# Optimization experiments

Hardware: AMD Instinct MI355X
Metric: run time of the kernel (lower is better)

Reference implementation:

```python
import jax, jax.numpy as jnp
import numpy as np

B, T, F, N = 262144, 3, 17, 8
EMBD = 32
DT = 0.2  # 25/5*0.04
EPS = 1e-8  # torch.cosine_similarity eps


def _mono(x, wi, bi, wo, bo):
    # monotonic_fun with increasing=False: relu(-Linear(x)) -> Linear
    h = jax.nn.relu(-(x @ wi.T + bi))  # (..., EMBD)
    return h @ wo.T + bo               # (..., 1)


def _cos(a, b):
    dot = jnp.sum(a * b, axis=-1)
    na = jnp.maximum(jnp.linalg.norm(a, axis=-1), EPS)
    nb = jnp.maximum(jnp.linalg.norm(b, axis=-1), EPS)
    return dot / (na * nb)


def _angle_clamp(vec, e, ang):
    # vec: (B,K,2), e: (B,2) -> keep forces within effective angle cone, sum over K
    keep = jnp.abs(_cos(e[:, None, :], vec)) > ang
    return jnp.sum(vec * keep[..., None], axis=1)


def setup_inputs() -> dict:
    key = jax.random.key(0)
    ks = jax.random.split(key, 8)
    ego = jax.random.normal(ks[0], (B, T, F), jnp.float32)
    ego = ego.at[:, :, 2:4].multiply(10.0)  # position scale
    nei = jax.random.normal(ks[1], (B, N, F), jnp.float32)
    nei = nei.at[:, :, 2:4].multiply(10.0).at[:, :, 4:6].multiply(0.1)
    border = jax.random.normal(ks[2], (4,), jnp.float32)
    attr_dest_para = jax.random.uniform(ks[3], (2,), jnp.float32) + 0.1  # relu(rand), keep away from 0 divisor
    eff_angle = jax.nn.sigmoid(jax.random.uniform(ks[4], (1,), jnp.float32))

    def mlp(k):
        k1, k2, k3, k4 = jax.random.split(k, 4)
        wi = jax.random.uniform(k1, (EMBD, 1), jnp.float32)      # clamped >= 0
        bi = jax.random.normal(k2, (EMBD,), jnp.float32) * 0.1
        wo = jax.random.uniform(k3, (1, EMBD), jnp.float32) * 0.1  # clamped >= 0
        bo = jax.random.normal(k4, (1,), jnp.float32) * 0.1
        return wi, bi, wo, bo

    an = mlp(ks[5])
    rn = mlp(ks[6])
    rb = mlp(ks[7])
    dl = mlp(jax.random.fold_in(key, 99))
    return dict(
        ego=ego, nei=nei, border=border,
        attr_dest_para=attr_dest_para, eff_angle=eff_angle,
        an_wi=an[0], an_bi=an[1], an_wo=an[2], an_bo=an[3],
        rn_wi=rn[0], rn_bi=rn[1], rn_wo=rn[2], rn_bo=rn[3],
        rb_wi=rb[0], rb_bi=rb[1], rb_wo=rb[2], rb_bo=rb[3],
        dl_wi=dl[0], dl_bi=dl[1], dl_wo=dl[2], dl_bo=dl[3],
    )


def reference(ego, nei, border, attr_dest_para, eff_angle,
              an_wi, an_bi, an_wo, an_bo,
              rn_wi, rn_bi, rn_wo, rn_bo,
              rb_wi, rb_bi, rb_wo, rb_bo,
              dl_wi, dl_bi, dl_wo, dl_bo):
    ego_last = ego[:, -1]  # (B,F)

    # --- attr_destination (desired_velocity=None branch) ---
    v34 = ego_last[:, 3:5]
    dv = jnp.stack([jnp.linalg.norm(v34, axis=-1),
                    jnp.zeros(ego.shape[0], ego.dtype)], axis=1)  # (B,2)
    f_dest = ((attr_dest_para[1] * dv - v34) / attr_dest_para[0])[:, None, :]  # (B,1,2)

    # --- attr_repu_neighbors ---
    r = nei[:, :, 2:4] - ego_last[:, None, 2:4]  # (B,N,2)
    mask = nei[:, :, 2:4] == 0                    # (B,N,2)
    r_norm = jnp.linalg.norm(r, axis=-1, keepdims=True)  # (B,N,1)

    # neighbor durality: quirky use of batch element 1, shared across batch
    ids_last = ego[1, -1, 8:-1]  # (8,) neighbor-id columns
    dur = jnp.zeros(N, ego.dtype)
    for t in range(ego.shape[1]):
        dur = dur + jnp.isin(ids_last, ego[1, t, 8:-1]).astype(ego.dtype)

    f_attr = _mono(r_norm, an_wi, an_bi, an_wo, an_bo) * r / r_norm \
             * _mono(dur[:, None], dl_wi, dl_bi, dl_wo, dl_bo)  # (B,N,2)*(N,1)
    f_attr = jnp.where(mask, 0.0, f_attr)

    v_nei = nei[:, :, 4:6]
    b = r_norm \
        + jnp.sum((r + v_nei * DT) ** 2, axis=-1, keepdims=True) \
        - jnp.sum((v_nei * DT) ** 2, axis=-1, keepdims=True)
    b = jnp.sqrt(b) / 2
    f_repu = _mono(b, rn_wi, rn_bi, rn_wo, rn_bo) * r / r_norm
    f_repu = jnp.where(mask, 0.0, f_repu)

    # --- repu_borders (select_lane = [0, -1]) ---
    rb_all = ego_last[:, 3, None] - border        # (B,4)
    rbv = jnp.stack([rb_all[:, 0], rb_all[:, -1]], axis=1)  # (B,2)
    rbn = jnp.abs(rbv)
    f_bor = _mono(rbn[..., None], rb_wi, rb_bi, rb_wo, rb_bo) * (rbv / rbn)[..., None]  # (B,2,1)
    f_bor = jnp.concatenate([jnp.zeros_like(f_bor), f_bor], axis=-1)  # (B,2,2): [0, fy]

    # --- angle clamp + integrate ---
    e = ego_last[:, 4:6]
    e = e / jnp.linalg.norm(e, axis=1, keepdims=True)
    a = (_angle_clamp(f_dest, e, eff_angle)
         + _angle_clamp(f_attr, e, eff_angle) + _angle_clamp(f_repu, e, eff_angle)
         + _angle_clamp(f_bor, e, eff_angle))
    v = ego_last[:, 2:4] + a * DT
    s = ego_last[:, :2] + v * DT
    return jnp.concatenate([s, v, a], axis=1)  # (B,6)
```

## Files before the change

### kernel.cpp

```cpp
#include <hip/hip_runtime.h>

#define DTC 0.2f
#define EPSC 1e-8f


__global__ __launch_bounds__(128) void sfm_pre(
    const float* __restrict__ ego,
    const float* __restrict__ an_wi, const float* __restrict__ an_bi, const float* __restrict__ an_wo,
    const float* __restrict__ rn_wi, const float* __restrict__ rn_bi, const float* __restrict__ rn_wo,
    const float* __restrict__ rb_wi, const float* __restrict__ rb_bi, const float* __restrict__ rb_wo,
    const float* __restrict__ dl_wi, const float* __restrict__ dl_bi,
    const float* __restrict__ dl_wo, const float* __restrict__ dl_bo,
    float* __restrict__ ws)
{
    __shared__ float tk[96], wiwo[96], wobi[96], skn[96], ssw[96], ssb[96];
    int t = threadIdx.x;
    if (t < 96) {
        int f = t >> 5, k = t & 31;
        const float* wip = (f == 0) ? an_wi : ((f == 1) ? rn_wi : rb_wi);
        const float* bip = (f == 0) ? an_bi : ((f == 1) ? rn_bi : rb_bi);
        const float* wop = (f == 0) ? an_wo : ((f == 1) ? rn_wo : rb_wo);
        float wi = wip[k], bi = bip[k], wo = wop[k];
        tk[t]   = -bi / wi;
        wiwo[t] = wi * wo;
        wobi[t] = wo * bi;
    }
    __syncthreads();
    if (t < 96) {
        int f = t >> 5, k = t & 31;
        float my = tk[t];
        int rank = 0;
        for (int m = 0; m < 32; ++m) {
            float o = tk[f * 32 + m];
            rank += (o < my || (o == my && m < k)) ? 1 : 0;
        }
        skn[f * 32 + rank] = my;
        ssw[f * 32 + rank] = wiwo[t];
        ssb[f * 32 + rank] = wobi[t];
    }
    __syncthreads();
    if (t < 96) {
        int f = t >> 5, p = t & 31;
        float sw_ = 0.f, sb_ = 0.f;
        for (int m = p; m < 32; ++m) { sw_ += ssw[f * 32 + m]; sb_ += ssb[f * 32 + m]; }
        int base = 16 + f * 112;
        ws[base + p]      = skn[f * 32 + p];
        ws[base + 32 + p] = sw_;
        ws[base + 65 + p] = sb_;
        if (p == 0) { ws[base + 64] = 0.f; ws[base + 97] = 0.f; }
    }
    if (t >= 96 && t < 104) {
        int j = t - 96;
        const float* base = ego + 51;
        float idv = base[2 * 17 + 8 + j];
        float dur = 0.f;
        for (int tt = 0; tt < 3; ++tt) {
            bool fo = false;
            for (int m = 0; m < 8; ++m) fo = fo || (idv == base[tt * 17 + 8 + m]);
            dur += fo ? 1.f : 0.f;
        }
        float acc = 0.f;
        for (int k = 0; k < 32; ++k)
            acc = fmaf(dl_wo[k], fmaxf(0.f, -fmaf(dl_wi[k], dur, dl_bi[k])), acc);
        ws[j] = acc + dl_bo[0];
    }
}

__device__ __forceinline__ float mono_eval(const float* __restrict__ kn, float x) {
    int i = (kn[15] <= x) ? 16 : 0;
    i += (kn[i + 7] <= x) ? 8 : 0;
    i += (kn[i + 3] <= x) ? 4 : 0;
    i += (kn[i + 1] <= x) ? 2 : 0;
    i += (kn[i] <= x) ? 1 : 0;
    return -fmaf(kn[32 + i], x, kn[65 + i]);
}

__global__ __launch_bounds__(256) void sfm_main(
    const float* __restrict__ ego, const float* __restrict__ nei,
    const float* __restrict__ border, const float* __restrict__ adp,
    const float* __restrict__ eang,
    const float* __restrict__ an_bo, const float* __restrict__ rn_bo,
    const float* __restrict__ rb_bo,
    const float* __restrict__ wsrc,
    float* __restrict__ out, int Bn)
{
    __shared__ float sw[360];
    int t = threadIdx.x;
    for (int i = t; i < 352; i += 256) sw[i] = wsrc[i];
    if (t == 0) sw[352] = an_bo[0];
    if (t == 1) sw[353] = rn_bo[0];
    if (t == 2) sw[354] = rb_bo[0];
    if (t == 3) sw[355] = adp[0];
    if (t == 4) sw[356] = adp[1];
    if (t == 5) sw[357] = eang[0];
    if (t == 6) sw[358] = border[0];
    if (t == 7) sw[359] = border[3];
    __syncthreads();

    int l = t & 7;
    long long row = (long long)blockIdx.x * 32 + (t >> 3);
    if (row >= Bn) return;

    float egv = 0.f;
    if (l < 6) egv = ego[row * 51 + 34 + l];
    int lb = (t & 63) & ~7;
    float g0 = __shfl(egv, lb + 0, 64);
    float g1 = __shfl(egv, lb + 1, 64);
    float g2 = __shfl(egv, lb + 2, 64);
    float g3 = __shfl(egv, lb + 3, 64);
    float g4 = __shfl(egv, lb + 4, 64);
    float g5 = __shfl(egv, lb + 5, 64);

    const float* nr = nei + row * 136 + l * 17 + 2;
    float nx = nr[0], ny = nr[1], vx = nr[2], vy = nr[3];

    float Rx = nx - g2, Ry = ny - g3;
    float rr = sqrtf(Rx * Rx + Ry * Ry);
    float ax = fmaf(vx, DTC, Rx), ay = fmaf(vy, DTC, Ry);
    float wx = vx * DTC, wy = vy * DTC;
    float bb = sqrtf(rr + ax * ax + ay * ay - wx * wx - wy * wy) * 0.5f;

    float an_bo_v = sw[352], rn_bo_v = sw[353], rb_bo_v = sw[354];
    float p0 = sw[355], p1 = sw[356], ang = sw[357];
    float rb0 = g3 - sw[358], rb1 = g3 - sw[359];
    float rbn0 = fabsf(rb0), rbn1 = fabsf(rb1);

    float fA = mono_eval(sw + 16, rr) + an_bo_v;
    float fR = mono_eval(sw + 128, bb) + rn_bo_v;
    float xb = (l == 1) ? rbn1 : rbn0;
    float vB = 0.f;
    if (l < 2) vB = mono_eval(sw + 240, xb) + rb_bo_v;
    float vB0 = __shfl(vB, lb + 0, 64);
    float vB1 = __shfl(vB, lb + 1, 64);

    float elen = sqrtf(g4 * g4 + g5 * g5);
    float ex = g4 / elen, ey = g5 / elen;
    float na = fmaxf(sqrtf(ex * ex + ey * ey), EPSC);

    float axs = 0.f, ays = 0.f;
#define CLAMP_ADD(VX, VY)                                                   \
    {                                                                       \
        float _vx = (VX), _vy = (VY);                                       \
        float _nv = fmaxf(sqrtf(_vx * _vx + _vy * _vy), EPSC);              \
        float _c = (ex * _vx + ey * _vy) / (na * _nv);                      \
        if (fabsf(_c) > ang) { axs += _vx; ays += _vy; }                    \
    }

    float mfx = (nx == 0.f) ? 0.f : 1.f;
    float mfy = (ny == 0.f) ? 0.f : 1.f;

    {
        float coef = fA / rr * sw[l];
        CLAMP_ADD(coef * Rx * mfx, coef * Ry * mfy);
    }
    {
        float coef = fR / rr;
        CLAMP_ADD(coef * Rx * mfx, coef * Ry * mfy);
    }

#pragma unroll
    for (int m = 1; m < 8; m <<= 1) {
        axs += __shfl_xor(axs, m, 64);
        ays += __shfl_xor(ays, m, 64);
    }

    if (l == 0) {
        float dvn = sqrtf(g3 * g3 + g4 * g4);
        CLAMP_ADD((p1 * dvn - g3) / p0, -g4 / p0);
        CLAMP_ADD(0.f, vB0 * (rb0 / rbn0));
        CLAMP_ADD(0.f, vB1 * (rb1 / rbn1));

        float vxo = fmaf(axs, DTC, g2);
        float vyo = fmaf(ays, DTC, g3);
        float* op = out + row * 6;
        op[0] = fmaf(vxo, DTC, g0);
        op[1] = fmaf(vyo, DTC, g1);
        op[2] = vxo; op[3] = vyo;
        op[4] = axs; op[5] = ays;
    }
#undef CLAMP_ADD
}

extern "C" void kernel_launch(void* const* d_in, const int* in_sizes, int n_in,
                              void* d_out, int out_size, void* d_ws, size_t ws_size,
                              hipStream_t stream) {
    const float* ego    = (const float*)d_in[0];
    const float* nei    = (const float*)d_in[1];
    const float* border = (const float*)d_in[2];
    const float* adp    = (const float*)d_in[3];
    const float* eang   = (const float*)d_in[4];
    const float* an_wi  = (const float*)d_in[5];
    const float* an_bi  = (const float*)d_in[6];
    const float* an_wo  = (const float*)d_in[7];
    const float* an_bo  = (const float*)d_in[8];
    const float* rn_wi  = (const float*)d_in[9];
    const float* rn_bi  = (const float*)d_in[10];
    const float* rn_wo  = (const float*)d_in[11];
    const float* rn_bo  = (const float*)d_in[12];
    const float* rb_wi  = (const float*)d_in[13];
    const float* rb_bi  = (const float*)d_in[14];
    const float* rb_wo  = (const float*)d_in[15];
    const float* rb_bo  = (const float*)d_in[16];
    const float* dl_wi  = (const float*)d_in[17];
    const float* dl_bi  = (const float*)d_in[18];
    const float* dl_wo  = (const float*)d_in[19];
    const float* dl_bo  = (const float*)d_in[20];
    float* out = (float*)d_out;
    float* ws  = (float*)d_ws;

    int Bn = in_sizes[0] / (3 * 17);

    sfm_pre<<<1, 128, 0, stream>>>(ego,
                                   an_wi, an_bi, an_wo,
                                   rn_wi, rn_bi, rn_wo,
                                   rb_wi, rb_bi, rb_wo,
                                   dl_wi, dl_bi, dl_wo, dl_bo, ws);

    int grid = (Bn + 31) / 32;
    sfm_main<<<grid, 256, 0, stream>>>(ego, nei, border, adp, eang,
                                       an_bo, rn_bo, rb_bo,
                                       ws, out, Bn);
}
```

Baseline: 278.8 us.

## Stage nei/ego tiles through LDS with coalesced float4 loads and coalesced output writes

```diff
diff --git a/kernel.cpp b/kernel.cpp
--- a/kernel.cpp
+++ b/kernel.cpp
@@ -85,7 +85,31 @@
     float* __restrict__ out, int Bn)
 {
     __shared__ float sw[360];
+    __shared__ float snei[4352];
+    __shared__ float sego[1632];
+    __shared__ float sout[192];
+
     int t = threadIdx.x;
+    long long blk = blockIdx.x;
+
+    {
+        const float4* nsrc = (const float4*)nei + blk * 1088;
+        long long ntot = (long long)Bn * 34;
+        float4* nd = (float4*)snei;
+#pragma unroll
+        for (int i = 0; i < 5; ++i) {
+            int idx = t + 256 * i;
+            if (idx < 1088 && blk * 1088 + idx < ntot) nd[idx] = nsrc[idx];
+        }
+        const float4* esrc = (const float4*)ego + blk * 408;
+        long long etot = (long long)Bn * 51 / 4;
+        float4* ed = (float4*)sego;
+#pragma unroll
+        for (int i = 0; i < 2; ++i) {
+            int idx = t + 256 * i;
+            if (idx < 408 && blk * 408 + idx < etot) ed[idx] = esrc[idx];
+        }
+    }
     for (int i = t; i < 352; i += 256) sw[i] = wsrc[i];
     if (t == 0) sw[352] = an_bo[0];
     if (t == 1) sw[353] = rn_bo[0];
@@ -97,21 +121,13 @@
     if (t == 7) sw[359] = border[3];
     __syncthreads();
 
-    int l = t & 7;
-    long long row = (long long)blockIdx.x * 32 + (t >> 3);
-    if (row >= Bn) return;
-
-    float egv = 0.f;
-    if (l < 6) egv = ego[row * 51 + 34 + l];
-    int lb = (t & 63) & ~7;
-    float g0 = __shfl(egv, lb + 0, 64);
-    float g1 = __shfl(egv, lb + 1, 64);
-    float g2 = __shfl(egv, lb + 2, 64);
-    float g3 = __shfl(egv, lb + 3, 64);
-    float g4 = __shfl(egv, lb + 4, 64);
-    float g5 = __shfl(egv, lb + 5, 64);
-
-    const float* nr = nei + row * 136 + l * 17 + 2;
+    int l  = t & 7;
+    int r32 = t >> 3;
+
+    const float* eg = sego + 51 * r32 + 34;
+    float g0 = eg[0], g1 = eg[1], g2 = eg[2], g3 = eg[3], g4 = eg[4], g5 = eg[5];
+
+    const float* nr = snei + 136 * r32 + 17 * l + 2;
     float nx = nr[0], ny = nr[1], vx = nr[2], vy = nr[3];
 
     float Rx = nx - g2, Ry = ny - g3;
@@ -130,6 +146,7 @@
     float xb = (l == 1) ? rbn1 : rbn0;
     float vB = 0.f;
     if (l < 2) vB = mono_eval(sw + 240, xb) + rb_bo_v;
+    int lb = (t & 63) & ~7;
     float vB0 = __shfl(vB, lb + 0, 64);
     float vB1 = __shfl(vB, lb + 1, 64);
 
@@ -172,13 +189,19 @@
 
         float vxo = fmaf(axs, DTC, g2);
         float vyo = fmaf(ays, DTC, g3);
-        float* op = out + row * 6;
+        float* op = sout + 6 * r32;
         op[0] = fmaf(vxo, DTC, g0);
         op[1] = fmaf(vyo, DTC, g1);
         op[2] = vxo; op[3] = vyo;
         op[4] = axs; op[5] = ays;
     }
 #undef CLAMP_ADD
+
+    __syncthreads();
+    if (t < 192) {
+        long long o = blk * 192 + t;
+        if (o < (long long)Bn * 6) out[o] = sout[t];
+    }
 }
 
 extern "C" void kernel_launch(void* const* d_in, const int* in_sizes, int n_in,
```

Measured after the change: 289.7 us. 3.9% more time.
